# Kernel optimization log

Measured on AMD Instinct MI355X. Metric: run time of the kernel, lower is better.

Reference implementation:

```python
import jax, jax.numpy as jnp
import numpy as np
from jax import lax

EPS = 1e-4


def setup_inputs() -> dict:
    key = jax.random.key(0)
    k1, k2, k3 = jax.random.split(key, 3)
    B, L, M, D = 4, 4096, 1024, 2048
    chunked_states = jax.random.normal(k1, (B, M, D), dtype=jnp.float32)
    boundary_prob = jax.random.uniform(k2, (B, L, 2), dtype=jnp.float32)
    boundary_mask = jax.random.randint(k3, (B, L), 0, 2).astype(jnp.bool_)
    return {
        "chunked_states": chunked_states,
        "boundary_prob": boundary_prob,
        "boundary_mask": boundary_mask,
    }


def _ema_scan(x, p):
    """out[0]=x[0]; out[t]=p[t]*x[t]+(1-p[t])*out[t-1] via associative scan.
    x: (B,M,D), p: (B,M)."""
    a = (1.0 - p).at[:, 0].set(0.0)                 # (B, M)
    b = (p[..., None] * x).at[:, 0].set(x[:, 0])    # (B, M, D)

    def combine(c1, c2):
        a1, b1 = c1
        a2, b2 = c2
        return a1 * a2, a2[..., None] * b1 + b2

    _, out = lax.associative_scan(combine, (a, b), axis=1)
    return out


def reference(chunked_states, boundary_prob, boundary_mask):
    B, L = boundary_mask.shape
    M, D = chunked_states.shape[1], chunked_states.shape[2]

    p = jnp.clip(boundary_prob[..., -1].astype(jnp.float32), EPS, 1.0 - EPS)  # (B, L)

    # Stable-in-effect sort: boundary tokens keep index, non-boundary shifted by +L
    token_idx = jnp.arange(L, dtype=jnp.int32)[None, :] + (~boundary_mask).astype(jnp.int32) * L
    sorted_indices = jnp.argsort(token_idx, axis=1)[:, :M]                    # (B, M)
    p_chunked = jnp.take_along_axis(p, sorted_indices, axis=1)                # (B, M)

    expanded_chunked = _ema_scan(chunked_states, p_chunked)                   # (B, M, D)

    chunk_indices = jnp.clip(jnp.cumsum(boundary_mask.astype(jnp.int32), axis=1) - 1, 0, M - 1)  # (B, L)
    expanded_states = jnp.take_along_axis(expanded_chunked, chunk_indices[..., None], axis=1)    # (B, L, D)
    return expanded_states
```

## Files before the change

kernel.cpp:

```cpp
#include <hip/hip_runtime.h>

#define BB 4
#define LL 4096
#define MM 1024
#define DD 2048
#define SEG 128
#define SM 8
#define NSCAN (BB * SEG * 2)
#define EXIT_EPS 1e-7f

typedef float f32x4 __attribute__((ext_vector_type(4)));

__global__ __launch_bounds__(1024) void prep_kernel(
    const float* __restrict__ bprob,
    const int*   __restrict__ bmask,
    float* __restrict__ p_chunked,
    int*   __restrict__ row_start,
    float* __restrict__ Pseg)
{
    const int b   = blockIdx.x;
    const int tid = threadIdx.x;
    const int lane = tid & 63;
    const int wid  = tid >> 6;

    __shared__ int wsum[16];
    __shared__ int s_total;
    __shared__ int rs_sh[MM + 1];

    rs_sh[tid] = LL;
    if (tid == 0) rs_sh[MM] = LL;

    int4 mv = reinterpret_cast<const int4*>(bmask + b * LL)[tid];
    int ms[4] = { mv.x, mv.y, mv.z, mv.w };
    int s = ms[0] + ms[1] + ms[2] + ms[3];

    int v = s;
    #pragma unroll
    for (int off = 1; off < 64; off <<= 1) {
        int u = __shfl_up(v, off, 64);
        if (lane >= off) v += u;
    }
    if (lane == 63) wsum[wid] = v;
    __syncthreads();
    if (tid == 0) {
        int acc = 0;
        #pragma unroll
        for (int w = 0; w < 16; ++w) { int t = wsum[w]; wsum[w] = acc; acc += t; }
        s_total = acc;
    }
    __syncthreads();

    const int NB = s_total;
    int e = (v - s) + wsum[wid];

    const int base_l = tid * 4;
    #pragma unroll
    for (int j = 0; j < 4; ++j) {
        int l = base_l + j;
        int m = ms[j];
        int incl = e + m;
        int ci = incl - 1;
        ci = ci < 0 ? 0 : (ci > MM - 1 ? MM - 1 : ci);
        int pci = e - 1;
        pci = pci < 0 ? 0 : (pci > MM - 1 ? MM - 1 : pci);
        if (l == 0 || ci != pci) rs_sh[ci] = l;
        int pos = m ? e : (NB + (l - e));
        if (pos < MM) {
            float2 pv = *reinterpret_cast<const float2*>(
                bprob + ((size_t)b * LL + l) * 2);
            float p = fminf(fmaxf(pv.y, 1e-4f), 1.0f - 1e-4f);
            p_chunked[b * MM + pos] = p;
        }
        e = incl;
    }
    __syncthreads();

    row_start[b * (MM + 1) + tid] = rs_sh[tid];
    if (tid == 0) row_start[b * (MM + 1) + MM] = rs_sh[MM];

    {
        int t = tid;
        float p = p_chunked[b * MM + t];
        float a = (t == 0) ? 0.0f : (1.0f - p);
        float pr = a;
        #pragma unroll
        for (int off = 1; off < SM; off <<= 1) {
            float u = __shfl_up(pr, off, SM);
            if ((t & (SM - 1)) >= off) pr *= u;
        }
        if ((t & (SM - 1)) == SM - 1) Pseg[b * SEG + (t >> 3)] = pr;
    }
}

__global__ __launch_bounds__(256) void seglast_kernel(
    const float* __restrict__ x,
    const float* __restrict__ p_chunked,
    float* __restrict__ seglast)
{
    const int tid = threadIdx.x;
    const int dsl = blockIdx.x;
    const int d0  = dsl * 1024 + tid * 4;
    const int seg = blockIdx.y;
    const int b   = blockIdx.z;
    const int t0  = seg * SM;

    __shared__ float sp[SM];
    if (tid < SM) sp[tid] = p_chunked[b * MM + t0 + tid];
    __syncthreads();

    const size_t base = ((size_t)b * MM + t0) * DD + d0;

    f32x4 prev = {0.0f, 0.0f, 0.0f, 0.0f};
    #pragma unroll
    for (int i = 0; i < SM; ++i) {
        float p = sp[i];
        float ac, bc;
        if (i == 0) { ac = (seg == 0) ? 0.0f : (1.0f - p); bc = (seg == 0) ? 1.0f : p; }
        else        { ac = 1.0f - p; bc = p; }
        f32x4 xt = *reinterpret_cast<const f32x4*>(x + base + (size_t)i * DD);
        prev = ac * prev + bc * xt;
    }
    *reinterpret_cast<f32x4*>(
        seglast + (((size_t)(b * 2 + dsl) * SEG + seg)) * 1024 + tid * 4) = prev;
}

static __device__ __forceinline__ f32x4 lookback(
    const float* __restrict__ seglast, const float* __restrict__ Pseg,
    int bd, int b, int seg, int tid)
{
    f32x4 c = {0.0f, 0.0f, 0.0f, 0.0f};
    float mult = 1.0f;
    const float* base = seglast + (size_t)bd * SEG * 1024 + tid * 4;
    for (int j = seg - 1; j >= 0; --j) {
        f32x4 sl = *reinterpret_cast<const f32x4*>(base + (size_t)j * 1024);
        c += mult * sl;
        mult *= Pseg[b * SEG + j];
        if (mult < EXIT_EPS) break;
    }
    return c;
}

__global__ __launch_bounds__(256) void scatter_kernel(
    const float* __restrict__ x,
    const float* __restrict__ p_chunked,
    const float* __restrict__ Pseg,
    const int*   __restrict__ row_start,
    const float* __restrict__ seglast,
    float* __restrict__ out)
{
    const int id  = blockIdx.x;
    const int tid = threadIdx.x;

    const int dsl = id & 1;
    const int seg = (id >> 1) & (SEG - 1);
    const int b   = id >> 8;
    const int d0  = dsl * 1024 + tid * 4;
    const int t0  = seg * SM;
    const int bd  = b * 2 + dsl;

    __shared__ float sp[SM];
    __shared__ int   rs[SM + 1];
    if (tid < SM) sp[tid] = p_chunked[b * MM + t0 + tid];
    if (tid < SM + 1) rs[tid] = row_start[b * (MM + 1) + t0 + tid];
    __syncthreads();

    f32x4 prev = lookback(seglast, Pseg, bd, b, seg, tid);

    const size_t base = ((size_t)b * MM + t0) * DD + d0;
    #pragma unroll
    for (int i = 0; i < SM; ++i) {
        float p = sp[i];
        float ac, bc;
        if (i == 0) { ac = (seg == 0) ? 0.0f : (1.0f - p); bc = (seg == 0) ? 1.0f : p; }
        else        { ac = 1.0f - p; bc = p; }
        f32x4 xt = *reinterpret_cast<const f32x4*>(x + base + (size_t)i * DD);
        prev = ac * prev + bc * xt;

        int t = t0 + i;
        if (t == MM - 1) continue;
        int l0r = rs[i], l1r = rs[i + 1];
        for (int l = l0r; l < l1r; ++l)
            *reinterpret_cast<f32x4*>(out + ((size_t)b * LL + l) * DD + d0) = prev;
    }

    {
        f32x4 v = lookback(seglast, Pseg, bd, b, SEG, tid);
        const int l0 = row_start[b * (MM + 1) + (MM - 1)];
        for (int l = l0 + seg; l < LL; l += SEG)
            *reinterpret_cast<f32x4*>(out + ((size_t)b * LL + l) * DD + d0) = v;
    }
}

extern "C" void kernel_launch(void* const* d_in, const int* in_sizes, int n_in,
                              void* d_out, int out_size, void* d_ws, size_t ws_size,
                              hipStream_t stream) {
    const float* x     = (const float*)d_in[0];
    const float* bprob = (const float*)d_in[1];
    const int*   bmask = (const int*)d_in[2];

    float* out = (float*)d_out;

    float* seglast   = (float*)d_ws;
    float* p_chunked = seglast + (size_t)BB * 2 * SEG * 1024;
    float* Pseg      = p_chunked + BB * MM;
    int*   row_start = (int*)(Pseg + BB * SEG);

    prep_kernel<<<BB, 1024, 0, stream>>>(bprob, bmask, p_chunked, row_start, Pseg);
    seglast_kernel<<<dim3(2, SEG, BB), 256, 0, stream>>>(x, p_chunked, seglast);
    scatter_kernel<<<NSCAN, 256, 0, stream>>>(
        x, p_chunked, Pseg, row_start, seglast, out);
}
```

Measured before the change: 43.41 us.

## Fuse prep into seglast kernel by recomputing per-batch prefix in each block

Removes the separate prep kernel and has every seglast block recompute the boundary-mask prefix sum, chunked probabilities, row starts and segment products in shared memory. One designated block per batch writes these to global memory for the scatter kernel. This removes one launch and the serial dependency on a 4-block prep kernel. The cost is redundant mask and probability reads and extra synchronisation in each of the seglast blocks.

```diff
diff --git a/kernel.cpp b/kernel.cpp
--- a/kernel.cpp
+++ b/kernel.cpp
@@ -11,28 +11,29 @@
 
 typedef float f32x4 __attribute__((ext_vector_type(4)));
 
-__global__ __launch_bounds__(1024) void prep_kernel(
-    const float* __restrict__ bprob,
-    const int*   __restrict__ bmask,
-    float* __restrict__ p_chunked,
-    int*   __restrict__ row_start,
-    float* __restrict__ Pseg)
-{
-    const int b   = blockIdx.x;
-    const int tid = threadIdx.x;
+static __device__ __forceinline__ void mini_prep(
+    const float* __restrict__ bprob, const int* __restrict__ bmask, int b,
+    float* spc, int* rs_sh, float* Pseg_sh, int* wsum)
+{
+    const int tid  = threadIdx.x;
     const int lane = tid & 63;
     const int wid  = tid >> 6;
 
-    __shared__ int wsum[16];
-    __shared__ int s_total;
-    __shared__ int rs_sh[MM + 1];
-
-    rs_sh[tid] = LL;
-    if (tid == 0) rs_sh[MM] = LL;
-
-    int4 mv = reinterpret_cast<const int4*>(bmask + b * LL)[tid];
-    int ms[4] = { mv.x, mv.y, mv.z, mv.w };
-    int s = ms[0] + ms[1] + ms[2] + ms[3];
+    for (int k = tid; k <= MM; k += 256) rs_sh[k] = LL;
+
+    int ms[16];
+    {
+        const int4* mp = reinterpret_cast<const int4*>(bmask + b * LL);
+        #pragma unroll
+        for (int k = 0; k < 4; ++k) {
+            int4 mv = mp[tid * 4 + k];
+            ms[k * 4 + 0] = mv.x; ms[k * 4 + 1] = mv.y;
+            ms[k * 4 + 2] = mv.z; ms[k * 4 + 3] = mv.w;
+        }
+    }
+    int s = 0;
+    #pragma unroll
+    for (int j = 0; j < 16; ++j) s += ms[j];
 
     int v = s;
     #pragma unroll
@@ -45,18 +46,16 @@
     if (tid == 0) {
         int acc = 0;
         #pragma unroll
-        for (int w = 0; w < 16; ++w) { int t = wsum[w]; wsum[w] = acc; acc += t; }
-        s_total = acc;
-    }
-    __syncthreads();
-
-    const int NB = s_total;
+        for (int w = 0; w < 4; ++w) { int t = wsum[w]; wsum[w] = acc; acc += t; }
+        wsum[4] = acc;
+    }
+    __syncthreads();
+    const int NB = wsum[4];
     int e = (v - s) + wsum[wid];
 
-    const int base_l = tid * 4;
-    #pragma unroll
-    for (int j = 0; j < 4; ++j) {
-        int l = base_l + j;
+    #pragma unroll
+    for (int j = 0; j < 16; ++j) {
+        int l = tid * 16 + j;
         int m = ms[j];
         int incl = e + m;
         int ci = incl - 1;
@@ -68,52 +67,59 @@
         if (pos < MM) {
             float2 pv = *reinterpret_cast<const float2*>(
                 bprob + ((size_t)b * LL + l) * 2);
-            float p = fminf(fmaxf(pv.y, 1e-4f), 1.0f - 1e-4f);
-            p_chunked[b * MM + pos] = p;
+            spc[pos] = fminf(fmaxf(pv.y, 1e-4f), 1.0f - 1e-4f);
         }
         e = incl;
     }
     __syncthreads();
 
-    row_start[b * (MM + 1) + tid] = rs_sh[tid];
-    if (tid == 0) row_start[b * (MM + 1) + MM] = rs_sh[MM];
-
-    {
-        int t = tid;
-        float p = p_chunked[b * MM + t];
-        float a = (t == 0) ? 0.0f : (1.0f - p);
-        float pr = a;
+    if (tid < SEG) {
+        float pr = 1.0f;
         #pragma unroll
-        for (int off = 1; off < SM; off <<= 1) {
-            float u = __shfl_up(pr, off, SM);
-            if ((t & (SM - 1)) >= off) pr *= u;
+        for (int i = 0; i < SM; ++i) {
+            int t = tid * SM + i;
+            float a = (t == 0) ? 0.0f : (1.0f - spc[t]);
+            pr *= a;
         }
-        if ((t & (SM - 1)) == SM - 1) Pseg[b * SEG + (t >> 3)] = pr;
-    }
+        Pseg_sh[tid] = pr;
+    }
+    __syncthreads();
 }
 
 __global__ __launch_bounds__(256) void seglast_kernel(
     const float* __restrict__ x,
-    const float* __restrict__ p_chunked,
-    float* __restrict__ seglast)
+    const float* __restrict__ bprob,
+    const int*   __restrict__ bmask,
+    float* __restrict__ seglast,
+    float* __restrict__ p_chunked,
+    int*   __restrict__ row_start,
+    float* __restrict__ Pseg)
 {
     const int tid = threadIdx.x;
     const int dsl = blockIdx.x;
-    const int d0  = dsl * 1024 + tid * 4;
     const int seg = blockIdx.y;
     const int b   = blockIdx.z;
+    const int d0  = dsl * 1024 + tid * 4;
     const int t0  = seg * SM;
 
-    __shared__ float sp[SM];
-    if (tid < SM) sp[tid] = p_chunked[b * MM + t0 + tid];
-    __syncthreads();
+    __shared__ float spc[MM];
+    __shared__ int   rs_sh[MM + 1];
+    __shared__ float Pseg_sh[SEG];
+    __shared__ int   wsum[5];
+
+    mini_prep(bprob, bmask, b, spc, rs_sh, Pseg_sh, wsum);
+
+    if (dsl == 0 && seg == 0) {
+        for (int k = tid; k < MM; k += 256) p_chunked[b * MM + k] = spc[k];
+        for (int k = tid; k <= MM; k += 256) row_start[b * (MM + 1) + k] = rs_sh[k];
+        if (tid < SEG) Pseg[b * SEG + tid] = Pseg_sh[tid];
+    }
 
     const size_t base = ((size_t)b * MM + t0) * DD + d0;
-
     f32x4 prev = {0.0f, 0.0f, 0.0f, 0.0f};
     #pragma unroll
     for (int i = 0; i < SM; ++i) {
-        float p = sp[i];
+        float p = spc[t0 + i];
         float ac, bc;
         if (i == 0) { ac = (seg == 0) ? 0.0f : (1.0f - p); bc = (seg == 0) ? 1.0f : p; }
         else        { ac = 1.0f - p; bc = p; }
@@ -205,8 +211,8 @@
     float* Pseg      = p_chunked + BB * MM;
     int*   row_start = (int*)(Pseg + BB * SEG);
 
-    prep_kernel<<<BB, 1024, 0, stream>>>(bprob, bmask, p_chunked, row_start, Pseg);
-    seglast_kernel<<<dim3(2, SEG, BB), 256, 0, stream>>>(x, p_chunked, seglast);
+    seglast_kernel<<<dim3(2, SEG, BB), 256, 0, stream>>>(
+        x, bprob, bmask, seglast, p_chunked, row_start, Pseg);
     scatter_kernel<<<NSCAN, 256, 0, stream>>>(
         x, p_chunked, Pseg, row_start, seglast, out);
 }
```

Result: slower. 44.51 us (+2.5%).
